# Kernel tuning notes

Measured on AMD Instinct MI355X. Metric: run time of the kernel, lower is better.

Reference implementation:

```python
import jax, jax.numpy as jnp
import numpy as np

N, T, D, K = 32, 8192, 64, 64
LOG2PI = float(np.log(2.0 * np.pi))


def setup_inputs() -> dict:
    key = jax.random.key(0)
    k1, k2, k3, k4 = jax.random.split(key, 4)
    x = jax.random.normal(k1, (N, T, D), dtype=jnp.float32)
    # valid GMM params: positive weights summing to 1, positive diagonal covariances
    weights = jax.nn.softmax(jax.random.normal(k2, (K,), dtype=jnp.float32))
    means = jax.random.normal(k3, (K, D), dtype=jnp.float32)
    covars = jax.random.uniform(k4, (K, D), dtype=jnp.float32, minval=0.5, maxval=1.5)
    return {"x": x, "weights": weights, "means": means, "covars": covars}


def _posterior(x, weights, means, covars):
    # diagonal-GMM predict_proba without materializing [N,T,K,D]:
    # sum_d (x-mu)^2/c = sum x^2/c - 2 sum x*mu/c + sum mu^2/c
    inv_c = 1.0 / covars                                   # [K,D]
    quad = (jnp.einsum('ntd,kd->ntk', x * x, inv_c)
            - 2.0 * jnp.einsum('ntd,kd->ntk', x, means * inv_c)
            + jnp.sum(means * means * inv_c, axis=-1))      # [N,T,K]
    log_prob = (jnp.log(weights)
                - 0.5 * (D * LOG2PI + jnp.sum(jnp.log(covars), axis=-1) + quad))
    return jax.nn.softmax(log_prob, axis=-1)               # [N,T,K]


def reference(x, weights, means, covars):
    # p = predict_proba * weights, renormalized over K (as in the torch code)
    p = _posterior(x, weights, means, covars) * weights
    p = p / jnp.sum(p, axis=-1, keepdims=True)             # [N,T,K]

    # pooled statistics over T (einsum avoids the [N,T,K,D] intermediate)
    s0 = jnp.sum(p, axis=1)                                # [N,K]
    s1 = jnp.einsum('ntk,ntd->nkd', p, x)                  # [N,K,D]
    s2 = jnp.einsum('ntk,ntd->nkd', p, x * x)              # [N,K,D]

    sw = jnp.sqrt(weights)                                 # [K]
    v0 = (s0 - T * weights) / sw                           # [N,K]
    v1 = (s1 - means * s0[..., None]) / (sw[:, None] * jnp.sqrt(covars))
    v2 = (s2 - 2.0 * means * s1 + (means ** 2 - covars) * s0[..., None]) / (
        jnp.sqrt(jnp.float32(2.0)) * sw[:, None] * covars)

    v = jnp.concatenate([v0[..., None], v1, v2], axis=2).reshape(x.shape[0], -1)
    # power normalization then L2 normalization
    v = jnp.sign(v) * jnp.sqrt(jnp.abs(v))
    v = v / jnp.linalg.norm(v, axis=1, keepdims=True)
    return v
```

## Files before the change

kernel.cpp:

```cpp
#include <hip/hip_runtime.h>
#include <math.h>

#define N_  32
#define T_  8192
#define D_  64
#define K_  64
#define CHUNKS 32
#define TOK_PER_BLOCK (T_ / CHUNKS)
#define TB 64
#define NBATCH (TOK_PER_BLOCK / TB)
#define STATS_PER_N (K_ + 2 * K_ * D_)
#define XSTR 72

typedef _Float16 half_t;
typedef __attribute__((ext_vector_type(8)))  _Float16 v8h;
typedef __attribute__((ext_vector_type(4)))  float    v4f;
typedef __attribute__((ext_vector_type(16))) float    v16f;

__global__ void prep_kernel(const float* __restrict__ w, const float* __restrict__ mu,
                            const float* __restrict__ cv, float* __restrict__ Ap,
                            half_t* __restrict__ WH, float* __restrict__ ssq) {
    if (blockIdx.x < 8) {
#pragma unroll
        for (int i = 0; i < 4; ++i) {
            const int e = blockIdx.x * 1024 + i * 256 + threadIdx.x;
            const int j = e & 7, l = (e >> 3) & 63, fs = e >> 9;
            const int tile = fs >> 2, s = fs & 3;
            const int kc = 16 * tile + (l & 15);
            const int f  = 32 * s + 8 * (l >> 4) + j;
            float val;
            if (f < 64) val = mu[kc * 64 + f] / cv[kc * 64 + f];
            else        val = -0.5f / cv[kc * 64 + (f - 64)];
            WH[e] = (half_t)val;
        }
    } else {
        if (threadIdx.x < 32) ssq[threadIdx.x] = 0.f;
        if (threadIdx.x < K_) {
            const int k = threadIdx.x;
            float acc = 0.f;
            for (int d = 0; d < D_; ++d) {
                const int idx = k * D_ + d;
                const float c = cv[idx], m = mu[idx];
                acc += logf(c) + m * m / c;
            }
            Ap[k] = 2.f * logf(w[k]) - 0.5f * acc;
        }
    }
}

__launch_bounds__(256, 3)
__global__ void main_kernel(const float* __restrict__ x, const float* __restrict__ Ap,
                            const half_t* __restrict__ WH, float* __restrict__ outbuf,
                            int mode) {
    __shared__ half_t Xs[TB][XSTR];
    __shared__ half_t Qs[TB][XSTR];
    __shared__ half_t Pt[K_][XSTR];
    __shared__ float  s0sh[4][64];

    const int tid  = threadIdx.x;
    const int lane = tid & 63;
    const int wv   = tid >> 6;
    const int chunk = blockIdx.x;
    const int n     = blockIdx.y;
    const int q     = lane >> 4;
    const int c0    = lane & 15;
    const int tok   = 16 * wv + c0;

    v8h Wf[16];
#pragma unroll
    for (int t = 0; t < 4; ++t)
#pragma unroll
        for (int s = 0; s < 4; ++s)
            Wf[t * 4 + s] = *(const v8h*)(WH + (size_t)((t * 4 + s) * 64 + lane) * 8);

    float apv[16];
#pragma unroll
    for (int t = 0; t < 4; ++t)
#pragma unroll
        for (int r = 0; r < 4; ++r) apv[t * 4 + r] = Ap[16 * t + 4 * q + r];

    float S0loc[16];
#pragma unroll
    for (int j = 0; j < 16; ++j) S0loc[j] = 0.f;

    const int sig = wv >> 1;
    const int dh  = wv & 1;
    v16f accB[2];
#pragma unroll
    for (int m = 0; m < 2; ++m)
#pragma unroll
        for (int r = 0; r < 16; ++r) accB[m][r] = 0.f;

    const size_t xbase = ((size_t)n * T_ + (size_t)chunk * TOK_PER_BLOCK) * (size_t)D_;
    const float* xrow0 = x + xbase + tok * 64 + 8 * q;

    float4 R[4];
    R[0] = *(const float4*)(xrow0);
    R[1] = *(const float4*)(xrow0 + 4);
    R[2] = *(const float4*)(xrow0 + 32);
    R[3] = *(const float4*)(xrow0 + 36);

#pragma unroll 1
    for (int batch = 0; batch < NBATCH; ++batch) {
        v8h xh0, xh1, qh0, qh1;
        {
            const float4 a = R[0], b = R[1], c = R[2], d = R[3];
            xh0[0] = (half_t)a.x; xh0[1] = (half_t)a.y; xh0[2] = (half_t)a.z; xh0[3] = (half_t)a.w;
            xh0[4] = (half_t)b.x; xh0[5] = (half_t)b.y; xh0[6] = (half_t)b.z; xh0[7] = (half_t)b.w;
            xh1[0] = (half_t)c.x; xh1[1] = (half_t)c.y; xh1[2] = (half_t)c.z; xh1[3] = (half_t)c.w;
            xh1[4] = (half_t)d.x; xh1[5] = (half_t)d.y; xh1[6] = (half_t)d.z; xh1[7] = (half_t)d.w;
            qh0[0] = (half_t)(a.x * a.x); qh0[1] = (half_t)(a.y * a.y);
            qh0[2] = (half_t)(a.z * a.z); qh0[3] = (half_t)(a.w * a.w);
            qh0[4] = (half_t)(b.x * b.x); qh0[5] = (half_t)(b.y * b.y);
            qh0[6] = (half_t)(b.z * b.z); qh0[7] = (half_t)(b.w * b.w);
            qh1[0] = (half_t)(c.x * c.x); qh1[1] = (half_t)(c.y * c.y);
            qh1[2] = (half_t)(c.z * c.z); qh1[3] = (half_t)(c.w * c.w);
            qh1[4] = (half_t)(d.x * d.x); qh1[5] = (half_t)(d.y * d.y);
            qh1[6] = (half_t)(d.z * d.z); qh1[7] = (half_t)(d.w * d.w);
            *(v8h*)&Xs[tok][8 * q]      = xh0;
            *(v8h*)&Xs[tok][32 + 8 * q] = xh1;
            *(v8h*)&Qs[tok][8 * q]      = qh0;
            *(v8h*)&Qs[tok][32 + 8 * q] = qh1;
        }

        if (batch + 1 < NBATCH) {
            const float* xr = xrow0 + (size_t)(batch + 1) * TB * D_;
            R[0] = *(const float4*)(xr);
            R[1] = *(const float4*)(xr + 4);
            R[2] = *(const float4*)(xr + 32);
            R[3] = *(const float4*)(xr + 36);
        }

        {
            v4f acc[4];
#pragma unroll
            for (int t = 0; t < 4; ++t) acc[t] = (v4f)(0.f);
#pragma unroll
            for (int t = 0; t < 4; ++t) {
                acc[t] = __builtin_amdgcn_mfma_f32_16x16x32_f16(Wf[t * 4 + 0], xh0, acc[t], 0, 0, 0);
                acc[t] = __builtin_amdgcn_mfma_f32_16x16x32_f16(Wf[t * 4 + 1], xh1, acc[t], 0, 0, 0);
                acc[t] = __builtin_amdgcn_mfma_f32_16x16x32_f16(Wf[t * 4 + 2], qh0, acc[t], 0, 0, 0);
                acc[t] = __builtin_amdgcn_mfma_f32_16x16x32_f16(Wf[t * 4 + 3], qh1, acc[t], 0, 0, 0);
            }
            float pv[16];
            float m = -1e30f;
#pragma unroll
            for (int t = 0; t < 4; ++t)
#pragma unroll
                for (int r = 0; r < 4; ++r) {
                    const float lg = acc[t][r] + apv[t * 4 + r];
                    pv[t * 4 + r] = lg;
                    m = fmaxf(m, lg);
                }
            m = fmaxf(m, __shfl_xor(m, 16, 64));
            m = fmaxf(m, __shfl_xor(m, 32, 64));
            float ssum = 0.f;
#pragma unroll
            for (int j = 0; j < 16; ++j) { pv[j] = __expf(pv[j] - m); ssum += pv[j]; }
            ssum += __shfl_xor(ssum, 16, 64);
            ssum += __shfl_xor(ssum, 32, 64);
            const float rs = 1.f / ssum;
#pragma unroll
            for (int j = 0; j < 16; ++j) { pv[j] *= rs; S0loc[j] += pv[j]; }
#pragma unroll
            for (int t = 0; t < 4; ++t)
#pragma unroll
                for (int r = 0; r < 4; ++r)
                    Pt[16 * t + 4 * q + r][tok] = (half_t)pv[t * 4 + r];
        }
        __syncthreads();

        {
            const half_t* Bsrc = (sig == 0) ? &Xs[0][0] : &Qs[0][0];
            const int m   = lane & 31;
            const int h   = lane >> 5;
            const int d   = 32 * dh + m;
            const half_t* Arow0 = &Pt[m][0];
            const half_t* Arow1 = &Pt[32 + m][0];
#pragma unroll
            for (int st = 0; st < 4; ++st) {
                const int tB = 16 * st + 8 * h;
                const v8h a0 = *(const v8h*)(Arow0 + tB);
                const v8h a1 = *(const v8h*)(Arow1 + tB);
                v8h bf;
#pragma unroll
                for (int j = 0; j < 8; ++j)
                    bf[j] = Bsrc[(tB + j) * XSTR + d];
                accB[0] = __builtin_amdgcn_mfma_f32_32x32x16_f16(a0, bf, accB[0], 0, 0, 0);
                accB[1] = __builtin_amdgcn_mfma_f32_32x32x16_f16(a1, bf, accB[1], 0, 0, 0);
            }
        }
        __syncthreads();
    }

#pragma unroll
    for (int j = 0; j < 16; ++j) {
        float v = S0loc[j];
        v += __shfl_xor(v, 1, 64);
        v += __shfl_xor(v, 2, 64);
        v += __shfl_xor(v, 4, 64);
        v += __shfl_xor(v, 8, 64);
        S0loc[j] = v;
    }
    if (c0 == 0) {
#pragma unroll
        for (int t = 0; t < 4; ++t)
#pragma unroll
            for (int r = 0; r < 4; ++r)
                s0sh[wv][16 * t + 4 * q + r] = S0loc[t * 4 + r];
    }
    __syncthreads();

    if (mode == 1) {
        float* dstb = outbuf + (size_t)(n * CHUNKS + chunk) * STATS_PER_N;
        if (tid < 64)
            dstb[tid] = s0sh[0][tid] + s0sh[1][tid] + s0sh[2][tid] + s0sh[3][tid];
        const int d = 32 * dh + (lane & 31);
        float* dst = dstb + 64 + sig * 4096;
#pragma unroll
        for (int mt = 0; mt < 2; ++mt)
#pragma unroll
            for (int r = 0; r < 16; ++r) {
                const int kc = 32 * mt + (r & 3) + 8 * (r >> 2) + 4 * (lane >> 5);
                dst[kc * 64 + d] = accB[mt][r];
            }
    } else {
        float* sb = outbuf + (size_t)n * STATS_PER_N;
        if (tid < 64)
            atomicAdd(&sb[tid], s0sh[0][tid] + s0sh[1][tid] + s0sh[2][tid] + s0sh[3][tid]);
        const int d = 32 * dh + (lane & 31);
        float* dst = sb + 64 + sig * 4096;
#pragma unroll
        for (int mt = 0; mt < 2; ++mt)
#pragma unroll
            for (int r = 0; r < 16; ++r) {
                const int kc = 32 * mt + (r & 3) + 8 * (r >> 2) + 4 * (lane >> 5);
                atomicAdd(&dst[kc * 64 + d], accB[mt][r]);
            }
    }
}

__global__ void reduce_pow_kernel(const float* __restrict__ partials,
                                  const float* __restrict__ w, const float* __restrict__ mu,
                                  const float* __restrict__ cv,
                                  float* __restrict__ us, float* __restrict__ ssq) {
    __shared__ float red[4];
    const int e = blockIdx.x * 256 + threadIdx.x;
    const int n = blockIdx.y;
    float u = 0.f;
    if (e < STATS_PER_N) {
        const float* base = partials + (size_t)n * CHUNKS * STATS_PER_N;
        float sv = 0.f;
#pragma unroll 8
        for (int c = 0; c < CHUNKS; ++c) sv += base[(size_t)c * STATS_PER_N + e];
        float v; int oidx;
        if (e < 64) {
            const float wv = w[e];
            v = (sv - (float)T_ * wv) * rsqrtf(wv);
            oidx = e * 129;
        } else if (e < 64 + 4096) {
            const int idx = e - 64, k = idx >> 6, d = idx & 63;
            float s0v = 0.f;
#pragma unroll 8
            for (int c = 0; c < CHUNKS; ++c) s0v += base[(size_t)c * STATS_PER_N + k];
            v = (sv - mu[idx] * s0v) * rsqrtf(w[k] * cv[idx]);
            oidx = k * 129 + 1 + d;
        } else {
            const int idx = e - 4160, k = idx >> 6, d = idx & 63;
            float s0v = 0.f, s1v = 0.f;
#pragma unroll 4
            for (int c = 0; c < CHUNKS; ++c) {
                s0v += base[(size_t)c * STATS_PER_N + k];
                s1v += base[(size_t)c * STATS_PER_N + 64 + idx];
            }
            const float m_ = mu[idx], c_ = cv[idx];
            v = (sv - 2.f * m_ * s1v + (m_ * m_ - c_) * s0v) * (rsqrtf(2.f * w[k]) / c_);
            oidx = k * 129 + 65 + d;
        }
        u = (v >= 0.f) ? sqrtf(v) : -sqrtf(-v);
        us[(size_t)n * STATS_PER_N + oidx] = u;
    }
    float ss = u * u;
#pragma unroll
    for (int off = 32; off > 0; off >>= 1) ss += __shfl_xor(ss, off, 64);
    if ((threadIdx.x & 63) == 0) red[threadIdx.x >> 6] = ss;
    __syncthreads();
    if (threadIdx.x == 0)
        atomicAdd(&ssq[n], red[0] + red[1] + red[2] + red[3]);
}

__global__ void scale_kernel(const float* __restrict__ us, const float* __restrict__ ssq,
                             float* __restrict__ out) {
    const int e = blockIdx.x * 256 + threadIdx.x;
    const int n = blockIdx.y;
    if (e < STATS_PER_N)
        out[(size_t)n * STATS_PER_N + e] = us[(size_t)n * STATS_PER_N + e] * rsqrtf(ssq[n]);
}

__global__ void fin_kernel(const float* __restrict__ w, const float* __restrict__ mu,
                           const float* __restrict__ cv, const float* __restrict__ stats,
                           float* __restrict__ out) {
    __shared__ float us[STATS_PER_N];
    __shared__ float red[4];
    const int n   = blockIdx.x;
    const int tid = threadIdx.x;
    const float* sb = stats + (size_t)n * STATS_PER_N;

    float ss = 0.f;
    if (tid < 64) {
        const float wv = w[tid];
        const float v = (sb[tid] - (float)T_ * wv) * rsqrtf(wv);
        const float u = (v >= 0.f) ? sqrtf(v) : -sqrtf(-v);
        us[tid * 129] = u;
        ss = fmaf(u, u, ss);
    }
#pragma unroll 1
    for (int i = 0; i < 16; ++i) {
        const int idx = i * 256 + tid;
        const int k = idx >> 6, d = idx & 63;
        const float v = (sb[64 + idx] - mu[idx] * sb[k]) * rsqrtf(w[k] * cv[idx]);
        const float u = (v >= 0.f) ? sqrtf(v) : -sqrtf(-v);
        us[k * 129 + 1 + d] = u;
        ss = fmaf(u, u, ss);
    }
#pragma unroll 1
    for (int i = 0; i < 16; ++i) {
        const int idx = i * 256 + tid;
        const int k = idx >> 6, d = idx & 63;
        const float m_ = mu[idx], c_ = cv[idx];
        const float s1v = sb[64 + idx], s2v = sb[64 + 4096 + idx];
        const float v = (s2v - 2.f * m_ * s1v + (m_ * m_ - c_) * sb[k]) *
                        (rsqrtf(2.f * w[k]) / c_);
        const float u = (v >= 0.f) ? sqrtf(v) : -sqrtf(-v);
        us[k * 129 + 65 + d] = u;
        ss = fmaf(u, u, ss);
    }
#pragma unroll
    for (int off = 32; off > 0; off >>= 1) ss += __shfl_xor(ss, off, 64);
    if ((tid & 63) == 0) red[tid >> 6] = ss;
    __syncthreads();
    const float tot = red[0] + red[1] + red[2] + red[3];
    const float rn = rsqrtf(tot);
    for (int e = tid; e < STATS_PER_N; e += 256)
        out[(size_t)n * STATS_PER_N + e] = us[e] * rn;
}

extern "C" void kernel_launch(void* const* d_in, const int* in_sizes, int n_in,
                              void* d_out, int out_size, void* d_ws, size_t ws_size,
                              hipStream_t stream) {
    const float* x  = (const float*)d_in[0];
    const float* w  = (const float*)d_in[1];
    const float* mu = (const float*)d_in[2];
    const float* cv = (const float*)d_in[3];
    float* out = (float*)d_out;

    const size_t part_elems = (size_t)CHUNKS * N_ * STATS_PER_N;
    const size_t us_elems   = (size_t)N_ * STATS_PER_N;
    const size_t need_big = (part_elems + us_elems + 32 + K_ + (size_t)K_ * 64) * sizeof(float);

    if (ws_size >= need_big) {
        float* partials = (float*)d_ws;
        float* us  = partials + part_elems;
        float* ssq = us + us_elems;
        float* Ap  = ssq + 32;
        half_t* WH = (half_t*)(Ap + K_);

        prep_kernel<<<9, 256, 0, stream>>>(w, mu, cv, Ap, WH, ssq);
        main_kernel<<<dim3(CHUNKS, N_), 256, 0, stream>>>(x, Ap, WH, partials, 1);
        reduce_pow_kernel<<<dim3(33, N_), 256, 0, stream>>>(partials, w, mu, cv, us, ssq);
        scale_kernel<<<dim3(33, N_), 256, 0, stream>>>(us, ssq, out);
    } else {
        float* stats = (float*)d_ws;
        float* ssq = stats + us_elems;
        float* Ap  = ssq + 32;
        half_t* WH = (half_t*)(Ap + K_);

        hipMemsetAsync(stats, 0, us_elems * sizeof(float), stream);
        prep_kernel<<<9, 256, 0, stream>>>(w, mu, cv, Ap, WH, ssq);
        main_kernel<<<dim3(CHUNKS, N_), 256, 0, stream>>>(x, Ap, WH, stats, 0);
        fin_kernel<<<N_, 256, 0, stream>>>(w, mu, cv, stats, out);
    }
}
```

Baseline: 154.2 us.

## Fuse chunk reduction and normalization into main kernel via last-block flag

The separate reduce_pow and scale kernels are dropped. Each main_kernel block now writes its partial statistics with agent-scope stores and bumps a per-sample counter, and the last block for each sample reduces all chunks, applies power and L2 normalization, and writes the output. The squared-x shared buffer Qs is also removed, with x^2 recomputed in registers from Xs in the second GEMM, which cuts shared memory and may raise occupancy. The cost is a serialized tail where one block per sample does the whole reduction, plus an atomic fence per block.

```diff
diff --git a/kernel.cpp b/kernel.cpp
--- a/kernel.cpp
+++ b/kernel.cpp
@@ -17,9 +17,16 @@
 typedef __attribute__((ext_vector_type(4)))  float    v4f;
 typedef __attribute__((ext_vector_type(16))) float    v16f;
 
+__device__ __forceinline__ void st_agent(float* p, float v) {
+    __hip_atomic_store(p, v, __ATOMIC_RELAXED, __HIP_MEMORY_SCOPE_AGENT);
+}
+__device__ __forceinline__ float ld_agent(const float* p) {
+    return __hip_atomic_load(p, __ATOMIC_RELAXED, __HIP_MEMORY_SCOPE_AGENT);
+}
+
 __global__ void prep_kernel(const float* __restrict__ w, const float* __restrict__ mu,
                             const float* __restrict__ cv, float* __restrict__ Ap,
-                            half_t* __restrict__ WH, float* __restrict__ ssq) {
+                            half_t* __restrict__ WH, int* __restrict__ flags) {
     if (blockIdx.x < 8) {
 #pragma unroll
         for (int i = 0; i < 4; ++i) {
@@ -34,7 +41,7 @@
             WH[e] = (half_t)val;
         }
     } else {
-        if (threadIdx.x < 32) ssq[threadIdx.x] = 0.f;
+        if (threadIdx.x < 32) flags[threadIdx.x] = 0;
         if (threadIdx.x < K_) {
             const int k = threadIdx.x;
             float acc = 0.f;
@@ -51,11 +58,21 @@
 __launch_bounds__(256, 3)
 __global__ void main_kernel(const float* __restrict__ x, const float* __restrict__ Ap,
                             const half_t* __restrict__ WH, float* __restrict__ outbuf,
-                            int mode) {
-    __shared__ half_t Xs[TB][XSTR];
-    __shared__ half_t Qs[TB][XSTR];
-    __shared__ half_t Pt[K_][XSTR];
-    __shared__ float  s0sh[4][64];
+                            float* __restrict__ out, int* __restrict__ flags,
+                            const float* __restrict__ w, const float* __restrict__ mu,
+                            const float* __restrict__ cv, int mode) {
+    __shared__ union {
+        struct {
+            half_t Xs[TB][XSTR];
+            half_t Pt[K_][XSTR];
+            float  s0sh[4][64];
+        } m;
+        struct {
+            float s0f[64];
+            float red[4];
+            int   lastflag;
+        } f;
+    } sm;
 
     const int tid  = threadIdx.x;
     const int lane = tid & 63;
@@ -117,10 +134,8 @@
             qh1[2] = (half_t)(c.z * c.z); qh1[3] = (half_t)(c.w * c.w);
             qh1[4] = (half_t)(d.x * d.x); qh1[5] = (half_t)(d.y * d.y);
             qh1[6] = (half_t)(d.z * d.z); qh1[7] = (half_t)(d.w * d.w);
-            *(v8h*)&Xs[tok][8 * q]      = xh0;
-            *(v8h*)&Xs[tok][32 + 8 * q] = xh1;
-            *(v8h*)&Qs[tok][8 * q]      = qh0;
-            *(v8h*)&Qs[tok][32 + 8 * q] = qh1;
+            *(v8h*)&sm.m.Xs[tok][8 * q]      = xh0;
+            *(v8h*)&sm.m.Xs[tok][32 + 8 * q] = xh1;
         }
 
         if (batch + 1 < NBATCH) {
@@ -166,17 +181,16 @@
             for (int t = 0; t < 4; ++t)
 #pragma unroll
                 for (int r = 0; r < 4; ++r)
-                    Pt[16 * t + 4 * q + r][tok] = (half_t)pv[t * 4 + r];
+                    sm.m.Pt[16 * t + 4 * q + r][tok] = (half_t)pv[t * 4 + r];
         }
         __syncthreads();
 
         {
-            const half_t* Bsrc = (sig == 0) ? &Xs[0][0] : &Qs[0][0];
-            const int m   = lane & 31;
+            const int mm  = lane & 31;
             const int h   = lane >> 5;
-            const int d   = 32 * dh + m;
-            const half_t* Arow0 = &Pt[m][0];
-            const half_t* Arow1 = &Pt[32 + m][0];
+            const int d   = 32 * dh + mm;
+            const half_t* Arow0 = &sm.m.Pt[mm][0];
+            const half_t* Arow1 = &sm.m.Pt[32 + mm][0];
 #pragma unroll
             for (int st = 0; st < 4; ++st) {
                 const int tB = 16 * st + 8 * h;
@@ -185,7 +199,8 @@
                 v8h bf;
 #pragma unroll
                 for (int j = 0; j < 8; ++j)
-                    bf[j] = Bsrc[(tB + j) * XSTR + d];
+                    bf[j] = sm.m.Xs[tB + j][d];
+                if (sig) bf = bf * bf;
                 accB[0] = __builtin_amdgcn_mfma_f32_32x32x16_f16(a0, bf, accB[0], 0, 0, 0);
                 accB[1] = __builtin_amdgcn_mfma_f32_32x32x16_f16(a1, bf, accB[1], 0, 0, 0);
             }
@@ -207,27 +222,99 @@
         for (int t = 0; t < 4; ++t)
 #pragma unroll
             for (int r = 0; r < 4; ++r)
-                s0sh[wv][16 * t + 4 * q + r] = S0loc[t * 4 + r];
+                sm.m.s0sh[wv][16 * t + 4 * q + r] = S0loc[t * 4 + r];
     }
     __syncthreads();
 
     if (mode == 1) {
         float* dstb = outbuf + (size_t)(n * CHUNKS + chunk) * STATS_PER_N;
         if (tid < 64)
-            dstb[tid] = s0sh[0][tid] + s0sh[1][tid] + s0sh[2][tid] + s0sh[3][tid];
-        const int d = 32 * dh + (lane & 31);
-        float* dst = dstb + 64 + sig * 4096;
-#pragma unroll
-        for (int mt = 0; mt < 2; ++mt)
-#pragma unroll
-            for (int r = 0; r < 16; ++r) {
-                const int kc = 32 * mt + (r & 3) + 8 * (r >> 2) + 4 * (lane >> 5);
-                dst[kc * 64 + d] = accB[mt][r];
-            }
+            st_agent(&dstb[tid],
+                     sm.m.s0sh[0][tid] + sm.m.s0sh[1][tid] + sm.m.s0sh[2][tid] + sm.m.s0sh[3][tid]);
+        {
+            const int d = 32 * dh + (lane & 31);
+            float* dst = dstb + 64 + sig * 4096;
+#pragma unroll
+            for (int mt = 0; mt < 2; ++mt)
+#pragma unroll
+                for (int r = 0; r < 16; ++r) {
+                    const int kc = 32 * mt + (r & 3) + 8 * (r >> 2) + 4 * (lane >> 5);
+                    st_agent(&dst[kc * 64 + d], accB[mt][r]);
+                }
+        }
+        __threadfence();
+        __syncthreads();
+        if (tid == 0) {
+            const int old = __hip_atomic_fetch_add(&flags[n], 1, __ATOMIC_ACQ_REL,
+                                                   __HIP_MEMORY_SCOPE_AGENT);
+            sm.f.lastflag = (old == CHUNKS - 1) ? 1 : 0;
+        }
+        __syncthreads();
+        if (!sm.f.lastflag) return;
+        __threadfence();
+
+        const float* Pn = outbuf + (size_t)n * CHUNKS * STATS_PER_N;
+        if (tid < 64) {
+            float a = 0.f;
+#pragma unroll
+            for (int c = 0; c < CHUNKS; ++c)
+                a += ld_agent(Pn + (size_t)c * STATS_PER_N + tid);
+            sm.f.s0f[tid] = a;
+        }
+        __syncthreads();
+
+        float* on = out + (size_t)n * STATS_PER_N;
+        float accs = 0.f;
+        float s1loc[16];
+#pragma unroll 1
+        for (int i = 0; i < 16; ++i) {
+            const int idx = i * 256 + tid;
+            float s1v = 0.f;
+#pragma unroll
+            for (int c = 0; c < CHUNKS; ++c)
+                s1v += ld_agent(Pn + (size_t)c * STATS_PER_N + 64 + idx);
+            s1loc[i] = s1v;
+            const int k = idx >> 6, d = idx & 63;
+            const float v = (s1v - mu[idx] * sm.f.s0f[k]) * rsqrtf(w[k] * cv[idx]);
+            const float u = (v >= 0.f) ? sqrtf(v) : -sqrtf(-v);
+            on[k * 129 + 1 + d] = u;
+            accs = fmaf(u, u, accs);
+        }
+        if (tid < 64) {
+            const float wv2 = w[tid];
+            const float v = (sm.f.s0f[tid] - (float)T_ * wv2) * rsqrtf(wv2);
+            const float u = (v >= 0.f) ? sqrtf(v) : -sqrtf(-v);
+            on[tid * 129] = u;
+            accs = fmaf(u, u, accs);
+        }
+#pragma unroll 1
+        for (int i = 0; i < 16; ++i) {
+            const int idx = i * 256 + tid;
+            float s2v = 0.f;
+#pragma unroll
+            for (int c = 0; c < CHUNKS; ++c)
+                s2v += ld_agent(Pn + (size_t)c * STATS_PER_N + 4160 + idx);
+            const int k = idx >> 6, d = idx & 63;
+            const float m_ = mu[idx], c_ = cv[idx];
+            const float v = (s2v - 2.f * m_ * s1loc[i] + (m_ * m_ - c_) * sm.f.s0f[k]) *
+                            (rsqrtf(2.f * w[k]) / c_);
+            const float u = (v >= 0.f) ? sqrtf(v) : -sqrtf(-v);
+            on[k * 129 + 65 + d] = u;
+            accs = fmaf(u, u, accs);
+        }
+        float ss = accs;
+#pragma unroll
+        for (int off = 32; off > 0; off >>= 1) ss += __shfl_xor(ss, off, 64);
+        if (lane == 0) sm.f.red[wv] = ss;
+        __syncthreads();
+        const float rn = rsqrtf(sm.f.red[0] + sm.f.red[1] + sm.f.red[2] + sm.f.red[3]);
+        for (int e = tid; e < STATS_PER_N; e += 256)
+            on[e] *= rn;
     } else {
         float* sb = outbuf + (size_t)n * STATS_PER_N;
         if (tid < 64)
-            atomicAdd(&sb[tid], s0sh[0][tid] + s0sh[1][tid] + s0sh[2][tid] + s0sh[3][tid]);
+            atomicAdd(&sb[tid],
+                      sm.m.s0sh[0][tid] + sm.m.s0sh[1][tid] + sm.m.s0sh[2][tid] + sm.m.s0sh[3][tid]);
         const int d = 32 * dh + (lane & 31);
         float* dst = sb + 64 + sig * 4096;
 #pragma unroll
@@ -238,63 +325,6 @@
                 atomicAdd(&dst[kc * 64 + d], accB[mt][r]);
             }
     }
-}
-
-__global__ void reduce_pow_kernel(const float* __restrict__ partials,
-                                  const float* __restrict__ w, const float* __restrict__ mu,
-                                  const float* __restrict__ cv,
-                                  float* __restrict__ us, float* __restrict__ ssq) {
-    __shared__ float red[4];
-    const int e = blockIdx.x * 256 + threadIdx.x;
-    const int n = blockIdx.y;
-    float u = 0.f;
-    if (e < STATS_PER_N) {
-        const float* base = partials + (size_t)n * CHUNKS * STATS_PER_N;
-        float sv = 0.f;
-#pragma unroll 8
-        for (int c = 0; c < CHUNKS; ++c) sv += base[(size_t)c * STATS_PER_N + e];
-        float v; int oidx;
-        if (e < 64) {
-            const float wv = w[e];
-            v = (sv - (float)T_ * wv) * rsqrtf(wv);
-            oidx = e * 129;
-        } else if (e < 64 + 4096) {
-            const int idx = e - 64, k = idx >> 6, d = idx & 63;
-            float s0v = 0.f;
-#pragma unroll 8
-            for (int c = 0; c < CHUNKS; ++c) s0v += base[(size_t)c * STATS_PER_N + k];
-            v = (sv - mu[idx] * s0v) * rsqrtf(w[k] * cv[idx]);
-            oidx = k * 129 + 1 + d;
-        } else {
-            const int idx = e - 4160, k = idx >> 6, d = idx & 63;
-            float s0v = 0.f, s1v = 0.f;
-#pragma unroll 4
-            for (int c = 0; c < CHUNKS; ++c) {
-                s0v += base[(size_t)c * STATS_PER_N + k];
-                s1v += base[(size_t)c * STATS_PER_N + 64 + idx];
-            }
-            const float m_ = mu[idx], c_ = cv[idx];
-            v = (sv - 2.f * m_ * s1v + (m_ * m_ - c_) * s0v) * (rsqrtf(2.f * w[k]) / c_);
-            oidx = k * 129 + 65 + d;
-        }
-        u = (v >= 0.f) ? sqrtf(v) : -sqrtf(-v);
-        us[(size_t)n * STATS_PER_N + oidx] = u;
-    }
-    float ss = u * u;
-#pragma unroll
-    for (int off = 32; off > 0; off >>= 1) ss += __shfl_xor(ss, off, 64);
-    if ((threadIdx.x & 63) == 0) red[threadIdx.x >> 6] = ss;
-    __syncthreads();
-    if (threadIdx.x == 0)
-        atomicAdd(&ssq[n], red[0] + red[1] + red[2] + red[3]);
-}
-
-__global__ void scale_kernel(const float* __restrict__ us, const float* __restrict__ ssq,
-                             float* __restrict__ out) {
-    const int e = blockIdx.x * 256 + threadIdx.x;
-    const int n = blockIdx.y;
-    if (e < STATS_PER_N)
-        out[(size_t)n * STATS_PER_N + e] = us[(size_t)n * STATS_PER_N + e] * rsqrtf(ssq[n]);
 }
 
 __global__ void fin_kernel(const float* __restrict__ w, const float* __restrict__ mu,
@@ -355,29 +385,29 @@
     float* out = (float*)d_out;
 
     const size_t part_elems = (size_t)CHUNKS * N_ * STATS_PER_N;
-    const size_t us_elems   = (size_t)N_ * STATS_PER_N;
-    const size_t need_big = (part_elems + us_elems + 32 + K_ + (size_t)K_ * 64) * sizeof(float);
+    const size_t need_big = (part_elems + 32 + K_) * sizeof(float) +
+                            (size_t)K_ * 128 * sizeof(half_t);
 
     if (ws_size >= need_big) {
         float* partials = (float*)d_ws;
-        float* us  = partials + part_elems;
-        float* ssq = us + us_elems;
-        float* Ap  = ssq + 32;
+        int*   flags = (int*)(partials + part_elems);
+        float* Ap  = (float*)(flags + 32);
         half_t* WH = (half_t*)(Ap + K_);
 
-        prep_kernel<<<9, 256, 0, stream>>>(w, mu, cv, Ap, WH, ssq);
-        main_kernel<<<dim3(CHUNKS, N_), 256, 0, stream>>>(x, Ap, WH, partials, 1);
-        reduce_pow_kernel<<<dim3(33, N_), 256, 0, stream>>>(partials, w, mu, cv, us, ssq);
-        scale_kernel<<<dim3(33, N_), 256, 0, stream>>>(us, ssq, out);
+        prep_kernel<<<9, 256, 0, stream>>>(w, mu, cv, Ap, WH, flags);
+        main_kernel<<<dim3(CHUNKS, N_), 256, 0, stream>>>(x, Ap, WH, partials, out,
+                                                          flags, w, mu, cv, 1);
     } else {
+        const size_t stats_elems = (size_t)N_ * STATS_PER_N;
         float* stats = (float*)d_ws;
-        float* ssq = stats + us_elems;
-        float* Ap  = ssq + 32;
+        int*   flags = (int*)(stats + stats_elems);
+        float* Ap  = (float*)(flags + 32);
         half_t* WH = (half_t*)(Ap + K_);
 
-        hipMemsetAsync(stats, 0, us_elems * sizeof(float), stream);
-        prep_kernel<<<9, 256, 0, stream>>>(w, mu, cv, Ap, WH, ssq);
-        main_kernel<<<dim3(CHUNKS, N_), 256, 0, stream>>>(x, Ap, WH, stats, 0);
+        hipMemsetAsync(stats, 0, stats_elems * sizeof(float), stream);
+        prep_kernel<<<9, 256, 0, stream>>>(w, mu, cv, Ap, WH, flags);
+        main_kernel<<<dim3(CHUNKS, N_), 256, 0, stream>>>(x, Ap, WH, stats, out,
+                                                          flags, w, mu, cv, 0);
         fin_kernel<<<N_, 256, 0, stream>>>(w, mu, cv, stats, out);
     }
 }
```

New measurement: 330.1 us. 114% more time.

## Double-buffer X and P tiles in LDS with one barrier per batch

Applied to the files above, without the earlier changes.

Restructures the batch loop into a software pipeline. Phase A (x conversion, posterior MFMA and softmax) for batch b+1 is written into the alternate LDS buffer while phase B (the P^T·X statistics MFMAs) consumes batch b, so each batch needs one __syncthreads instead of two. The separate Qs tile of x² is dropped: phase B squares the fp16 x values in registers, which saves LDS and stores but changes rounding slightly. Double buffering increases LDS use per block, which may affect occupancy.

```diff
diff --git a/kernel.cpp b/kernel.cpp
--- a/kernel.cpp
+++ b/kernel.cpp
@@ -52,9 +52,8 @@
 __global__ void main_kernel(const float* __restrict__ x, const float* __restrict__ Ap,
                             const half_t* __restrict__ WH, float* __restrict__ outbuf,
                             int mode) {
-    __shared__ half_t Xs[TB][XSTR];
-    __shared__ half_t Qs[TB][XSTR];
-    __shared__ half_t Pt[K_][XSTR];
+    __shared__ half_t Xs[2][TB][XSTR];
+    __shared__ half_t Pt[2][K_][XSTR];
     __shared__ float  s0sh[4][64];
 
     const int tid  = threadIdx.x;
@@ -100,8 +99,8 @@
     R[2] = *(const float4*)(xrow0 + 32);
     R[3] = *(const float4*)(xrow0 + 36);
 
-#pragma unroll 1
-    for (int batch = 0; batch < NBATCH; ++batch) {
+    auto phaseA = [&](int i) {
+        const int buf = i & 1;
         v8h xh0, xh1, qh0, qh1;
         {
             const float4 a = R[0], b = R[1], c = R[2], d = R[3];
@@ -117,80 +116,81 @@
             qh1[2] = (half_t)(c.z * c.z); qh1[3] = (half_t)(c.w * c.w);
             qh1[4] = (half_t)(d.x * d.x); qh1[5] = (half_t)(d.y * d.y);
             qh1[6] = (half_t)(d.z * d.z); qh1[7] = (half_t)(d.w * d.w);
-            *(v8h*)&Xs[tok][8 * q]      = xh0;
-            *(v8h*)&Xs[tok][32 + 8 * q] = xh1;
-            *(v8h*)&Qs[tok][8 * q]      = qh0;
-            *(v8h*)&Qs[tok][32 + 8 * q] = qh1;
-        }
-
-        if (batch + 1 < NBATCH) {
-            const float* xr = xrow0 + (size_t)(batch + 1) * TB * D_;
+            *(v8h*)&Xs[buf][tok][8 * q]      = xh0;
+            *(v8h*)&Xs[buf][tok][32 + 8 * q] = xh1;
+        }
+        if (i + 1 < NBATCH) {
+            const float* xr = xrow0 + (size_t)(i + 1) * TB * D_;
             R[0] = *(const float4*)(xr);
             R[1] = *(const float4*)(xr + 4);
             R[2] = *(const float4*)(xr + 32);
             R[3] = *(const float4*)(xr + 36);
         }
-
-        {
-            v4f acc[4];
-#pragma unroll
-            for (int t = 0; t < 4; ++t) acc[t] = (v4f)(0.f);
-#pragma unroll
-            for (int t = 0; t < 4; ++t) {
-                acc[t] = __builtin_amdgcn_mfma_f32_16x16x32_f16(Wf[t * 4 + 0], xh0, acc[t], 0, 0, 0);
-                acc[t] = __builtin_amdgcn_mfma_f32_16x16x32_f16(Wf[t * 4 + 1], xh1, acc[t], 0, 0, 0);
-                acc[t] = __builtin_amdgcn_mfma_f32_16x16x32_f16(Wf[t * 4 + 2], qh0, acc[t], 0, 0, 0);
-                acc[t] = __builtin_amdgcn_mfma_f32_16x16x32_f16(Wf[t * 4 + 3], qh1, acc[t], 0, 0, 0);
-            }
-            float pv[16];
-            float m = -1e30f;
-#pragma unroll
-            for (int t = 0; t < 4; ++t)
-#pragma unroll
-                for (int r = 0; r < 4; ++r) {
-                    const float lg = acc[t][r] + apv[t * 4 + r];
-                    pv[t * 4 + r] = lg;
-                    m = fmaxf(m, lg);
-                }
-            m = fmaxf(m, __shfl_xor(m, 16, 64));
-            m = fmaxf(m, __shfl_xor(m, 32, 64));
-            float ssum = 0.f;
-#pragma unroll
-            for (int j = 0; j < 16; ++j) { pv[j] = __expf(pv[j] - m); ssum += pv[j]; }
-            ssum += __shfl_xor(ssum, 16, 64);
-            ssum += __shfl_xor(ssum, 32, 64);
-            const float rs = 1.f / ssum;
-#pragma unroll
-            for (int j = 0; j < 16; ++j) { pv[j] *= rs; S0loc[j] += pv[j]; }
-#pragma unroll
-            for (int t = 0; t < 4; ++t)
-#pragma unroll
-                for (int r = 0; r < 4; ++r)
-                    Pt[16 * t + 4 * q + r][tok] = (half_t)pv[t * 4 + r];
-        }
+        v4f acc[4];
+#pragma unroll
+        for (int t = 0; t < 4; ++t) acc[t] = (v4f)(0.f);
+#pragma unroll
+        for (int t = 0; t < 4; ++t) {
+            acc[t] = __builtin_amdgcn_mfma_f32_16x16x32_f16(Wf[t * 4 + 0], xh0, acc[t], 0, 0, 0);
+            acc[t] = __builtin_amdgcn_mfma_f32_16x16x32_f16(Wf[t * 4 + 1], xh1, acc[t], 0, 0, 0);
+            acc[t] = __builtin_amdgcn_mfma_f32_16x16x32_f16(Wf[t * 4 + 2], qh0, acc[t], 0, 0, 0);
+            acc[t] = __builtin_amdgcn_mfma_f32_16x16x32_f16(Wf[t * 4 + 3], qh1, acc[t], 0, 0, 0);
+        }
+        float pv[16];
+        float m = -1e30f;
+#pragma unroll
+        for (int t = 0; t < 4; ++t)
+#pragma unroll
+            for (int r = 0; r < 4; ++r) {
+                const float lg = acc[t][r] + apv[t * 4 + r];
+                pv[t * 4 + r] = lg;
+                m = fmaxf(m, lg);
+            }
+        m = fmaxf(m, __shfl_xor(m, 16, 64));
+        m = fmaxf(m, __shfl_xor(m, 32, 64));
+        float ssum = 0.f;
+#pragma unroll
+        for (int j = 0; j < 16; ++j) { pv[j] = __expf(pv[j] - m); ssum += pv[j]; }
+        ssum += __shfl_xor(ssum, 16, 64);
+        ssum += __shfl_xor(ssum, 32, 64);
+        const float rs = 1.f / ssum;
+#pragma unroll
+        for (int j = 0; j < 16; ++j) { pv[j] *= rs; S0loc[j] += pv[j]; }
+#pragma unroll
+        for (int t = 0; t < 4; ++t)
+#pragma unroll
+            for (int r = 0; r < 4; ++r)
+                Pt[buf][16 * t + 4 * q + r][tok] = (half_t)pv[t * 4 + r];
+    };
+
+    auto phaseB = [&](int i) {
+        const int buf = i & 1;
+        const int mm  = lane & 31;
+        const int h   = lane >> 5;
+        const int d   = 32 * dh + mm;
+        const half_t* Arow0 = &Pt[buf][mm][0];
+        const half_t* Arow1 = &Pt[buf][32 + mm][0];
+#pragma unroll
+        for (int st = 0; st < 4; ++st) {
+            const int tB = 16 * st + 8 * h;
+            const v8h a0 = *(const v8h*)(Arow0 + tB);
+            const v8h a1 = *(const v8h*)(Arow1 + tB);
+            v8h bf;
+#pragma unroll
+            for (int j = 0; j < 8; ++j)
+                bf[j] = Xs[buf][tB + j][d];
+            if (sig) bf = bf * bf;
+            accB[0] = __builtin_amdgcn_mfma_f32_32x32x16_f16(a0, bf, accB[0], 0, 0, 0);
+            accB[1] = __builtin_amdgcn_mfma_f32_32x32x16_f16(a1, bf, accB[1], 0, 0, 0);
+        }
+    };
+
+    phaseA(0);
+#pragma unroll 1
+    for (int b = 0; b < NBATCH; ++b) {
         __syncthreads();
-
-        {
-            const half_t* Bsrc = (sig == 0) ? &Xs[0][0] : &Qs[0][0];
-            const int m   = lane & 31;
-            const int h   = lane >> 5;
-            const int d   = 32 * dh + m;
-            const half_t* Arow0 = &Pt[m][0];
-            const half_t* Arow1 = &Pt[32 + m][0];
-#pragma unroll
-            for (int st = 0; st < 4; ++st) {
-                const int tB = 16 * st + 8 * h;
-                const v8h a0 = *(const v8h*)(Arow0 + tB);
-                const v8h a1 = *(const v8h*)(Arow1 + tB);
-                v8h bf;
-#pragma unroll
-                for (int j = 0; j < 8; ++j)
-                    bf[j] = Bsrc[(tB + j) * XSTR + d];
-                accB[0] = __builtin_amdgcn_mfma_f32_32x32x16_f16(a0, bf, accB[0], 0, 0, 0);
-                accB[1] = __builtin_amdgcn_mfma_f32_32x32x16_f16(a1, bf, accB[1], 0, 0, 0);
-            }
-        }
-        __syncthreads();
+        if (b + 1 < NBATCH) phaseA(b + 1);
+        phaseB(b);
     }
 
 #pragma unroll
```

After: 158.4 us. 1.03x slower.
